# Performance work log

Measured on AMD Instinct MI355X. Metric: run time of the kernel, lower is better.

Reference implementation:

```python
import jax, jax.numpy as jnp
import numpy as np

NEG_SLOPE = 0.2

def _lrelu(x):
    return jax.nn.leaky_relu(x, NEG_SLOPE)

def _seg_mean(vals, seg_ids, num_segments):
    # scatter-mean: sum per segment / count (count clamped to 1 -> zeros for empty nodes,
    # matching torch version where untouched nodes keep new_x == 0)
    s = jax.ops.segment_sum(vals, seg_ids, num_segments=num_segments)
    c = jax.ops.segment_sum(jnp.ones((vals.shape[0], 1), vals.dtype), seg_ids, num_segments=num_segments)
    return s / jnp.maximum(c, 1.0)

def _messages(x, src, dst, rel, ts, rel_emb, time_emb, W_rt, b_rt, W_fc, b_fc):
    # MessagePassing.forward: rel_e = lrelu(rel_t_trans(cat(rel_e, time_e)));
    # m = lrelu(fc(cat(x[src], rel_e, x[dst])))
    rel_e = _lrelu(jnp.concatenate([rel_emb[rel], time_emb[ts]], axis=-1) @ W_rt + b_rt)  # [E, 2h]
    m = _lrelu(jnp.concatenate([x[src], rel_e, x[dst]], axis=-1) @ W_fc + b_fc)           # [E, 2h]
    return m

def setup_inputs() -> dict:
    key = jax.random.key(0)
    ks = jax.random.split(key, 16)
    N, F, H, E, B = 20000, 128, 64, 200000, 256
    NUM_REL, NUM_TS, MAX_ENT = 200, 365, 5000
    s = 0.05
    inp = {}
    inp['x_feat'] = jax.random.normal(ks[0], (N, F), jnp.float32)
    inp['node_grp_emb'] = jax.random.normal(ks[1], (MAX_ENT, H), jnp.float32) * s
    inp['rel_emb'] = jax.random.normal(ks[2], (NUM_REL, H), jnp.float32) * s
    # TimeEncode (TGAT-style fixed frequencies): cos(t * 1/10^(linspace(0,9,H)))
    t = jnp.arange(NUM_TS, dtype=jnp.float32)
    freq = 1.0 / (10.0 ** jnp.linspace(0.0, 9.0, H, dtype=jnp.float32))
    inp['time_emb'] = jnp.cos(t[:, None] * freq[None, :])
    inp['W_node'] = jax.random.normal(ks[3], (F, H), jnp.float32) * s
    inp['b_node'] = jnp.zeros((H,), jnp.float32)
    inp['W_rt'] = jax.random.normal(ks[4], (2 * H, 2 * H), jnp.float32) * s
    inp['b_rt'] = jnp.zeros((2 * H,), jnp.float32)
    inp['W_fc'] = jax.random.normal(ks[5], (6 * H, 2 * H), jnp.float32) * s
    inp['b_fc'] = jnp.zeros((2 * H,), jnp.float32)
    inp['w_pred'] = jax.random.normal(ks[6], (6 * H, 1), jnp.float32) * s
    inp['b_pred'] = jnp.zeros((1,), jnp.float32)
    inp['node_ent'] = jax.random.randint(ks[7], (N,), 0, MAX_ENT)
    inp['edge_src'] = jax.random.randint(ks[8], (E,), 0, N)
    inp['edge_dst'] = jax.random.randint(ks[9], (E,), 0, N)
    inp['edge_type'] = jax.random.randint(ks[10], (E,), 0, NUM_REL)
    inp['edge_ts'] = jax.random.randint(ks[11], (E,), 0, NUM_TS)
    inp['q_s'] = jax.random.randint(ks[12], (B,), 0, N)
    inp['q_o'] = jax.random.randint(ks[13], (B,), 0, N)
    inp['q_r'] = jax.random.randint(ks[14], (B,), 0, NUM_REL)
    inp['q_t'] = jax.random.randint(ks[15], (B,), 0, NUM_TS)
    inp['num_hops'] = 2
    return inp

def reference(x_feat, node_grp_emb, rel_emb, time_emb, W_node, b_node, W_rt, b_rt,
              W_fc, b_fc, w_pred, b_pred, node_ent, edge_src, edge_dst, edge_type,
              edge_ts, q_s, q_o, q_r, q_t, num_hops):
    N = x_feat.shape[0]
    # node init: x = cat(lrelu(node_emb(feat)), node_grp_emb[ent])  (dropout = eval identity)
    x = jnp.concatenate([_lrelu(x_feat @ W_node + b_node), node_grp_emb[node_ent]], axis=-1)  # [N, 2h]
    # multi-hop gather -> edge MLP -> scatter-mean (frontier loop flattened to num_hops full passes)
    for _ in range(num_hops):
        m = _messages(x, edge_src, edge_dst, edge_type, edge_ts, rel_emb, time_emb, W_rt, b_rt, W_fc, b_fc)
        x = x + _seg_mean(m, edge_dst, N)
    # final aggregation only into query destination nodes q_o
    m = _messages(x, edge_src, edge_dst, edge_type, edge_ts, rel_emb, time_emb, W_rt, b_rt, W_fc, b_fc)
    agg = _seg_mean(m, edge_dst, N)
    qo_mask = jnp.zeros((N, 1), x.dtype).at[q_o].set(1.0)
    x = x + agg * qo_mask
    # query relation/time transform and prediction
    q_r_t = _lrelu(jnp.concatenate([rel_emb[q_r], time_emb[q_t]], axis=-1) @ W_rt + b_rt)  # [B, 2h]
    final_feat = jnp.concatenate([x[q_s], q_r_t, x[q_o]], axis=-1)                          # [B, 6h]
    out = jax.nn.sigmoid(final_feat @ w_pred + b_pred)
    return out.squeeze(-1)
```

## Files before the change

### kernel.cpp

```cpp
#include <hip/hip_runtime.h>
#include <cstddef>
#include <cstdint>

#define H 64
#define TWOH 128
#define LRELU(v) ((v) >= 0.f ? (v) : 0.2f * (v))

typedef __attribute__((ext_vector_type(4))) float f32x4;
typedef __attribute__((ext_vector_type(8))) short bf16x8;

__device__ inline unsigned short f2bf(float f) {
    union { float f; unsigned u; } v; v.f = f;
    unsigned u = v.u + 0x7FFFu + ((v.u >> 16) & 1u);
    return (unsigned short)(u >> 16);
}
__device__ inline float bf2f(unsigned u16) {
    union { unsigned u; float f; } v; v.u = u16 << 16; return v.f;
}

__global__ __launch_bounds__(256) void k_setup(
    const float* __restrict__ xf, const float* __restrict__ grp,
    const float* __restrict__ Wn, const float* __restrict__ bn,
    const int* __restrict__ ent, float* __restrict__ x, unsigned short* __restrict__ xb,
    const float* __restrict__ Wfc, unsigned short* __restrict__ WT,
    const float* __restrict__ rel_emb, const float* __restrict__ time_emb,
    const float* __restrict__ Wrt, const float* __restrict__ brt,
    const int* __restrict__ qr, const int* __restrict__ qt,
    float* __restrict__ AR, float* __restrict__ BT, float* __restrict__ qrt,
    const int* __restrict__ dst, int* deg,
    int N, int E, int B, int NUM_REL, int NUM_TS,
    int NB_NI, int NB_TW, int NB_RT)
{
    int b = blockIdx.x, t = threadIdx.x;
    __shared__ float s_u[32][128];
    if (b < NB_NI) {
        int n0 = b * 32;
        int w = t >> 6, l = t & 63;
#pragma unroll
        for (int i = 0; i < 4; ++i) {
            int idx = t + i * 256; int r = idx >> 5, c4 = (idx & 31) * 4;
            int n = n0 + r;
            float4 v = make_float4(0.f, 0.f, 0.f, 0.f);
            if (n < N) v = *(const float4*)(xf + (size_t)n * 128 + c4);
            *(float4*)(&s_u[r][c4]) = v;
        }
        __syncthreads();
        float acc[8];
#pragma unroll
        for (int r = 0; r < 8; ++r) acc[r] = 0.f;
        for (int k = 0; k < 128; ++k) {
            float wv = Wn[k * H + l];
#pragma unroll
            for (int r = 0; r < 8; ++r) acc[r] += s_u[w * 8 + r][k] * wv;
        }
        float bb = bn[l];
        for (int r = 0; r < 8; ++r) {
            int n = n0 + w * 8 + r; if (n >= N) break;
            float v = LRELU(acc[r] + bb);
            float g = grp[(size_t)ent[n] * H + l];
            x[(size_t)n * TWOH + l]      = v;
            x[(size_t)n * TWOH + H + l]  = g;
            xb[(size_t)n * TWOH + l]     = f2bf(v);
            xb[(size_t)n * TWOH + H + l] = f2bf(g);
        }
    } else if (b < NB_NI + NB_TW) {
        int tid = (b - NB_NI) * 256 + t;
        int m = tid >> 14, rem = tid & 16383, col = rem >> 7, k = rem & 127;
        WT[(size_t)m * 16384 + col * 128 + k] = f2bf(Wfc[((size_t)m * 128 + k) * 128 + col]);
    } else if (b < NB_NI + NB_TW + NB_RT) {
        int sub = t >> 7, tt = t & 127;
        int row = (b - NB_NI - NB_TW) * 2 + sub;
        int RT_ROWS = NUM_REL + NUM_TS + B;
        int valid = row < RT_ROWS;
        int type = 0, ridx = 0;
        if (valid) {
            if (row < NUM_REL)               { type = 0; ridx = row; }
            else if (row < NUM_REL + NUM_TS) { type = 1; ridx = row - NUM_REL; }
            else                             { type = 2; ridx = row - NUM_REL - NUM_TS; }
        }
        float lv = 0.f;
        if (valid) {
            if (type == 0)      lv = (tt < H) ? rel_emb[(size_t)ridx * H + tt] : 0.f;
            else if (type == 1) lv = (tt >= H) ? time_emb[(size_t)ridx * H + (tt - H)] : 0.f;
            else                lv = (tt < H) ? rel_emb[(size_t)qr[ridx] * H + tt]
                                              : time_emb[(size_t)qt[ridx] * H + (tt - H)];
        }
        s_u[sub][tt] = lv;
        __syncthreads();
        if (valid) {
            float acc = 0.f;
            for (int k = 0; k < 128; ++k) acc += s_u[sub][k] * Wrt[(size_t)k * TWOH + tt];
            if (type != 1) acc += brt[tt];
            if (type == 2) acc = LRELU(acc);
            if (type == 0)      AR[(size_t)ridx * TWOH + tt]  = acc;
            else if (type == 1) BT[(size_t)ridx * TWOH + tt]  = acc;
            else                qrt[(size_t)ridx * TWOH + tt] = acc;
        }
    } else {
        int e = (b - NB_NI - NB_TW - NB_RT) * 256 + t;
        if (e < E) atomicAdd(&deg[dst[e]], 1);
    }
}

__global__ __launch_bounds__(1024) void k_scan(const int* __restrict__ deg,
                                               int* __restrict__ curs, int N)
{
    __shared__ int wpre[17];
    __shared__ int carry;
    int t = (int)threadIdx.x, wave = t >> 6, lane = t & 63;
    if (t == 0) carry = 0;
    __syncthreads();
    for (int base = 0; base < N; base += 1024) {
        int i = base + t;
        int v = (i < N) ? deg[i] : 0;
        int sv = v;
#pragma unroll
        for (int off = 1; off < 64; off <<= 1) {
            int u = __shfl_up(sv, off);
            if (lane >= off) sv += u;
        }
        if (lane == 63) wpre[wave + 1] = sv;
        __syncthreads();
        if (t == 0) {
            wpre[0] = 0;
            for (int w = 1; w <= 16; ++w) wpre[w] += wpre[w - 1];
        }
        __syncthreads();
        if (i < N) curs[i] = carry + wpre[wave] + sv - v;
        __syncthreads();
        if (t == 0) carry += wpre[16];
        __syncthreads();
    }
}

__global__ __launch_bounds__(256) void k_mid2(
    const float* __restrict__ AR, const float* __restrict__ BT,
    const unsigned short* __restrict__ WT, const float* __restrict__ bd,
    unsigned short* __restrict__ RE2b, int NC, int NUM_TS,
    const unsigned short* __restrict__ xb,
    unsigned short* __restrict__ XSb, unsigned short* __restrict__ XDb, int N,
    const int* __restrict__ src, const int* __restrict__ dst,
    const int* __restrict__ etype, const int* __restrict__ ets,
    int* cursor, int2* __restrict__ a_sc, int E,
    const int* __restrict__ qo, int* maski, int* __restrict__ qlist, int* cntQ, int B,
    int NB_RE2, int NB_G, int NB_SC)
{
    __shared__ __align__(16) char smem[33280];
    int b = blockIdx.x, t = threadIdx.x;
    if (b < NB_RE2) {
        unsigned short* s_mid = (unsigned short*)smem;
        unsigned short* s_out = (unsigned short*)(smem + 16384);
        int* s_rel = (int*)(smem + 32768);
        int* s_ts  = s_rel + 64;
        const unsigned short* WTr = WT + 16384;
        int c0 = b * 64;
        if (t < 64) {
            int cc = c0 + t; if (cc >= NC) cc = NC - 1;
            int rel = cc / NUM_TS;
            s_rel[t] = rel; s_ts[t] = cc - rel * NUM_TS;
        }
        __syncthreads();
#pragma unroll
        for (int i = 0; i < 4; ++i) {
            int idx = t + i * 256;
            int r = idx >> 4, c8 = (idx & 15) * 8;
            const float* ar = AR + (size_t)s_rel[r] * TWOH + c8;
            const float* bt = BT + (size_t)s_ts[r]  * TWOH + c8;
            unsigned short tmp[8] __attribute__((aligned(16)));
#pragma unroll
            for (int j = 0; j < 8; ++j) {
                float v = ar[j] + bt[j];
                tmp[j] = f2bf(LRELU(v));
            }
            int byte = r * 256 + ((c8 * 2) ^ ((r & 7) << 4));
            *(bf16x8*)(smem + byte) = *(bf16x8*)tmp;
        }
        __syncthreads();
        int w = t >> 6, l = t & 63;
        int arow = w * 16 + (l & 15);
        int kgrp = (l >> 4) * 8;
        f32x4 acc[8];
#pragma unroll
        for (int ct = 0; ct < 8; ++ct) acc[ct] = (f32x4){0.f, 0.f, 0.f, 0.f};
#pragma unroll
        for (int kc = 0; kc < 128; kc += 32) {
            int kb = (kc + kgrp) * 2;
            bf16x8 a = *(bf16x8*)((char*)s_mid + arow * 256 + (kb ^ ((arow & 7) << 4)));
#pragma unroll
            for (int ct = 0; ct < 8; ++ct) {
                bf16x8 bb = *(const bf16x8*)(WTr + (size_t)(ct * 16 + (l & 15)) * TWOH + kc + kgrp);
                acc[ct] = __builtin_amdgcn_mfma_f32_16x16x32_bf16(a, bb, acc[ct], 0, 0, 0);
            }
        }
#pragma unroll
        for (int ct = 0; ct < 8; ++ct) {
#pragma unroll
            for (int reg = 0; reg < 4; ++reg) {
                int row  = w * 16 + (l >> 4) * 4 + reg;
                int colb = (ct * 16 + (l & 15)) * 2;
                *(unsigned short*)((char*)s_out + row * 256 + (colb ^ ((row & 7) << 4)))
                    = f2bf(acc[ct][reg]);
            }
        }
        __syncthreads();
#pragma unroll
        for (int i = 0; i < 4; ++i) {
            int idx = t + i * 256;
            int r = idx >> 4, c16 = (idx & 15) * 16;
            int cc = c0 + r;
            if (cc >= NC) continue;
            bf16x8 v = *(bf16x8*)((char*)s_out + r * 256 + (c16 ^ ((r & 7) << 4)));
            *(bf16x8*)(RE2b + (size_t)cc * TWOH + c16 / 2) = v;
        }
    } else if (b < NB_RE2 + NB_G) {
        unsigned short* s_oS = (unsigned short*)smem;
        unsigned short* s_oD = (unsigned short*)(smem + 8192);
        int bid = b - NB_RE2;
        int n0 = (bid >> 1) * 64;
        int colbase = (bid & 1) * 64;
        const unsigned short* WTs = WT;
        const unsigned short* WTd = WT + 32768;
        int w = t >> 6, l = t & 63;
        int node = n0 + w * 16 + (l & 15); if (node >= N) node = N - 1;
        int kgrp = (l >> 4) * 8;
        f32x4 aS[4], aD[4];
#pragma unroll
        for (int ct = 0; ct < 4; ++ct) { aS[ct] = (f32x4){0.f,0.f,0.f,0.f}; aD[ct] = (f32x4){0.f,0.f,0.f,0.f}; }
#pragma unroll
        for (int kc = 0; kc < 128; kc += 32) {
            bf16x8 a = *(const bf16x8*)(xb + (size_t)node * TWOH + kc + kgrp);
#pragma unroll
            for (int ct = 0; ct < 4; ++ct) {
                size_t wo = (size_t)(colbase + ct * 16 + (l & 15)) * TWOH + kc + kgrp;
                bf16x8 b1 = *(const bf16x8*)(WTs + wo);
                bf16x8 b2 = *(const bf16x8*)(WTd + wo);
                aS[ct] = __builtin_amdgcn_mfma_f32_16x16x32_bf16(a, b1, aS[ct], 0, 0, 0);
                aD[ct] = __builtin_amdgcn_mfma_f32_16x16x32_bf16(a, b2, aD[ct], 0, 0, 0);
            }
        }
#pragma unroll
        for (int ct = 0; ct < 4; ++ct) {
            int lc = ct * 16 + (l & 15);
            float bb = bd[colbase + lc];
#pragma unroll
            for (int reg = 0; reg < 4; ++reg) {
                int row = w * 16 + (l >> 4) * 4 + reg;
                int off = row * 128 + ((lc * 2) ^ ((row & 7) << 4));
                *(unsigned short*)((char*)s_oS + off) = f2bf(aS[ct][reg]);
                *(unsigned short*)((char*)s_oD + off) = f2bf(aD[ct][reg] + bb);
            }
        }
        __syncthreads();
#pragma unroll
        for (int i = 0; i < 2; ++i) {
            int idx = t + i * 256;
            int r = idx >> 3, c16 = (idx & 7) * 16;
            int n = n0 + r; if (n >= N) continue;
            int off = r * 128 + (c16 ^ ((r & 7) << 4));
            *(bf16x8*)(XSb + (size_t)n * TWOH + colbase + c16 / 2) = *(bf16x8*)((char*)s_oS + off);
            *(bf16x8*)(XDb + (size_t)n * TWOH + colbase + c16 / 2) = *(bf16x8*)((char*)s_oD + off);
        }
    } else if (b < NB_RE2 + NB_G + NB_SC) {
        int e = (b - NB_RE2 - NB_G) * 256 + t;
        if (e < E) {
            int pos = atomicAdd(&cursor[dst[e]], 1);
            a_sc[pos] = make_int2(src[e], etype[e] * NUM_TS + ets[e]);
        }
    } else {
        for (int i = t; i < B; i += 256) {
            int n = qo[i];
            if (atomicExch(&maski[n], 1) == 0) qlist[atomicAdd(cntQ, 1)] = n;
        }
    }
}

__global__ __launch_bounds__(256) void k_gemm_dual_mfma(
    const unsigned short* __restrict__ xb,
    const unsigned short* __restrict__ WTs, const unsigned short* __restrict__ WTd,
    const float* __restrict__ bd,
    unsigned short* __restrict__ XSb, unsigned short* __restrict__ XDb, int M)
{
    __shared__ unsigned short s_oS[64 * 64];
    __shared__ unsigned short s_oD[64 * 64];
    int t  = threadIdx.x;
    int n0 = blockIdx.x * 64;
    int colbase = blockIdx.y * 64;
    int w = t >> 6, l = t & 63;
    int node = n0 + w * 16 + (l & 15); if (node >= M) node = M - 1;
    int kgrp = (l >> 4) * 8;
    f32x4 aS[4], aD[4];
#pragma unroll
    for (int ct = 0; ct < 4; ++ct) { aS[ct] = (f32x4){0.f,0.f,0.f,0.f}; aD[ct] = (f32x4){0.f,0.f,0.f,0.f}; }
#pragma unroll
    for (int kc = 0; kc < 128; kc += 32) {
        bf16x8 a = *(const bf16x8*)(xb + (size_t)node * TWOH + kc + kgrp);
#pragma unroll
        for (int ct = 0; ct < 4; ++ct) {
            size_t wo = (size_t)(colbase + ct * 16 + (l & 15)) * TWOH + kc + kgrp;
            bf16x8 b1 = *(const bf16x8*)(WTs + wo);
            bf16x8 b2 = *(const bf16x8*)(WTd + wo);
            aS[ct] = __builtin_amdgcn_mfma_f32_16x16x32_bf16(a, b1, aS[ct], 0, 0, 0);
            aD[ct] = __builtin_amdgcn_mfma_f32_16x16x32_bf16(a, b2, aD[ct], 0, 0, 0);
        }
    }
#pragma unroll
    for (int ct = 0; ct < 4; ++ct) {
        int lc = ct * 16 + (l & 15);
        float bb = bd[colbase + lc];
#pragma unroll
        for (int reg = 0; reg < 4; ++reg) {
            int row = w * 16 + (l >> 4) * 4 + reg;
            int off = row * 128 + ((lc * 2) ^ ((row & 7) << 4));
            *(unsigned short*)((char*)s_oS + off) = f2bf(aS[ct][reg]);
            *(unsigned short*)((char*)s_oD + off) = f2bf(aD[ct][reg] + bb);
        }
    }
    __syncthreads();
#pragma unroll
    for (int i = 0; i < 2; ++i) {
        int idx = t + i * 256;
        int r = idx >> 3, c16 = (idx & 7) * 16;
        int n = n0 + r; if (n >= M) continue;
        int off = r * 128 + (c16 ^ ((r & 7) << 4));
        *(bf16x8*)(XSb + (size_t)n * TWOH + colbase + c16 / 2) = *(bf16x8*)((char*)s_oS + off);
        *(bf16x8*)(XDb + (size_t)n * TWOH + colbase + c16 / 2) = *(bf16x8*)((char*)s_oD + off);
    }
}

__global__ __launch_bounds__(256) void k_gemm_list(
    const unsigned short* __restrict__ xb, const unsigned short* __restrict__ WT,
    const float* __restrict__ bd,
    const int* __restrict__ listS, const int* __restrict__ cntS,
    const int* __restrict__ qlist, const int* __restrict__ cntQ,
    unsigned short* __restrict__ XSb, unsigned short* __restrict__ XDb)
{
    int mode = blockIdx.y;
    const int* list = mode ? qlist : listS;
    int c = mode ? *cntQ : *cntS;
    int r0 = blockIdx.x * 64;
    if (r0 >= c) return;
    const unsigned short* W = mode ? (WT + 32768) : WT;
    unsigned short* Out = mode ? XDb : XSb;

    __shared__ unsigned short s_out[64 * 128];
    int t = threadIdx.x;
    int w = t >> 6, l = t & 63;
    int slot = r0 + w * 16 + (l & 15); if (slot >= c) slot = c - 1;
    int node = list[slot];
    int kgrp = (l >> 4) * 8;
    f32x4 acc[8];
#pragma unroll
    for (int ct = 0; ct < 8; ++ct) acc[ct] = (f32x4){0.f, 0.f, 0.f, 0.f};
#pragma unroll
    for (int kc = 0; kc < 128; kc += 32) {
        bf16x8 a = *(const bf16x8*)(xb + (size_t)node * TWOH + kc + kgrp);
#pragma unroll
        for (int ct = 0; ct < 8; ++ct) {
            bf16x8 b = *(const bf16x8*)(W + (size_t)(ct * 16 + (l & 15)) * TWOH + kc + kgrp);
            acc[ct] = __builtin_amdgcn_mfma_f32_16x16x32_bf16(a, b, acc[ct], 0, 0, 0);
        }
    }
#pragma unroll
    for (int ct = 0; ct < 8; ++ct) {
        int col = ct * 16 + (l & 15);
        float bb = mode ? bd[col] : 0.f;
#pragma unroll
        for (int reg = 0; reg < 4; ++reg) {
            int row = w * 16 + (l >> 4) * 4 + reg;
            int off = row * 256 + ((col * 2) ^ ((row & 7) << 4));
            *(unsigned short*)((char*)s_out + off) = f2bf(acc[ct][reg] + bb);
        }
    }
    __syncthreads();
#pragma unroll
    for (int i = 0; i < 4; ++i) {
        int idx = t + i * 256;
        int r = idx >> 4, c16 = (idx & 15) * 16;
        if (r0 + r >= c) continue;
        int n = list[r0 + r];
        bf16x8 v = *(bf16x8*)((char*)s_out + r * 256 + (c16 ^ ((r & 7) << 4)));
        *(bf16x8*)(Out + (size_t)n * TWOH + c16 / 2) = v;
    }
}

__global__ __launch_bounds__(256) void k_agg(
    float* __restrict__ x, unsigned short* __restrict__ xb,
    const unsigned short* __restrict__ XSb, const unsigned short* __restrict__ XDb,
    const unsigned short* __restrict__ RE2b,
    const int* __restrict__ cursor, const int* __restrict__ deg,
    const int2* __restrict__ a_sc,
    const int* __restrict__ list, const int* __restrict__ cnt, int N,
    int nAggBlk, const int* __restrict__ qlistM, const int* __restrict__ cntQM,
    int* maskS, int* __restrict__ listS, int* cntS)
{
    if ((int)blockIdx.x >= nAggBlk) {
        int slot = ((int)blockIdx.x - nAggBlk) * 4 + (threadIdx.x >> 6);
        if (slot >= *cntQM) return;
        int n = qlistM[slot];
        int lane = threadIdx.x & 63;
        int end = cursor[n], start = end - deg[n];
        for (int p = start + lane; p < end; p += 64) {
            int s = a_sc[p].x;
            if (atomicExch(&maskS[s], 1) == 0) listS[atomicAdd(cntS, 1)] = s;
        }
        return;
    }
    int slot = blockIdx.x * 4 + (threadIdx.x >> 6);
    int n;
    if (list) {
        if (slot >= *cnt) return;
        n = list[slot];
    } else {
        n = slot; if (n >= N) return;
    }
    int lane = threadIdx.x & 63;
    int col  = lane * 2;
    int d    = deg[n];
    int end  = cursor[n], start = end - d;
    unsigned cvu = *(const unsigned*)(XDb + (size_t)n * TWOH + col);
    float cvx = bf2f(cvu & 0xFFFFu), cvy = bf2f(cvu >> 16);
    float ax = 0.f, ay = 0.f;
    for (int base = start; base < end; base += 64) {
        int m = end - base; if (m > 64) m = 64;
        int2 my = make_int2(0, 0);
        if (base + lane < end) my = a_sc[base + lane];
        int j = 0;
        for (; j + 4 <= m; j += 4) {
            int s0 = __shfl(my.x, j),     c0 = __shfl(my.y, j);
            int s1 = __shfl(my.x, j + 1), c1 = __shfl(my.y, j + 1);
            int s2 = __shfl(my.x, j + 2), c2 = __shfl(my.y, j + 2);
            int s3 = __shfl(my.x, j + 3), c3 = __shfl(my.y, j + 3);
            unsigned u0 = *(const unsigned*)(XSb  + (size_t)s0 * TWOH + col);
            unsigned v0 = *(const unsigned*)(RE2b + (size_t)c0 * TWOH + col);
            unsigned u1 = *(const unsigned*)(XSb  + (size_t)s1 * TWOH + col);
            unsigned v1 = *(const unsigned*)(RE2b + (size_t)c1 * TWOH + col);
            unsigned u2 = *(const unsigned*)(XSb  + (size_t)s2 * TWOH + col);
            unsigned v2 = *(const unsigned*)(RE2b + (size_t)c2 * TWOH + col);
            unsigned u3 = *(const unsigned*)(XSb  + (size_t)s3 * TWOH + col);
            unsigned v3 = *(const unsigned*)(RE2b + (size_t)c3 * TWOH + col);
            float m0 = bf2f(u0 & 0xFFFFu) + bf2f(v0 & 0xFFFFu) + cvx; m0 = LRELU(m0);
            float m1 = bf2f(u0 >> 16)     + bf2f(v0 >> 16)     + cvy; m1 = LRELU(m1);
            float m2 = bf2f(u1 & 0xFFFFu) + bf2f(v1 & 0xFFFFu) + cvx; m2 = LRELU(m2);
            float m3 = bf2f(u1 >> 16)     + bf2f(v1 >> 16)     + cvy; m3 = LRELU(m3);
            float m4 = bf2f(u2 & 0xFFFFu) + bf2f(v2 & 0xFFFFu) + cvx; m4 = LRELU(m4);
            float m5 = bf2f(u2 >> 16)     + bf2f(v2 >> 16)     + cvy; m5 = LRELU(m5);
            float m6 = bf2f(u3 & 0xFFFFu) + bf2f(v3 & 0xFFFFu) + cvx; m6 = LRELU(m6);
            float m7 = bf2f(u3 >> 16)     + bf2f(v3 >> 16)     + cvy; m7 = LRELU(m7);
            ax += (m0 + m2) + (m4 + m6); ay += (m1 + m3) + (m5 + m7);
        }
        for (; j < m; ++j) {
            int s0 = __shfl(my.x, j), c0 = __shfl(my.y, j);
            unsigned u0 = *(const unsigned*)(XSb  + (size_t)s0 * TWOH + col);
            unsigned v0 = *(const unsigned*)(RE2b + (size_t)c0 * TWOH + col);
            float m0 = bf2f(u0 & 0xFFFFu) + bf2f(v0 & 0xFFFFu) + cvx; m0 = LRELU(m0);
            float m1 = bf2f(u0 >> 16)     + bf2f(v0 >> 16)     + cvy; m1 = LRELU(m1);
            ax += m0; ay += m1;
        }
    }
    float inv = 1.f / (float)(d > 1 ? d : 1);
    float* xr = x + (size_t)n * TWOH + col;
    float nx = xr[0] + ax * inv, ny = xr[1] + ay * inv;
    xr[0] = nx; xr[1] = ny;
    *(unsigned*)(xb + (size_t)n * TWOH + col) = ((unsigned)f2bf(ny) << 16) | f2bf(nx);
}

__global__ __launch_bounds__(64) void k_predict(
    const float* __restrict__ x, const float* __restrict__ qrt,
    const float* __restrict__ wp, const float* __restrict__ bp,
    const int* __restrict__ qs, const int* __restrict__ qo,
    float* __restrict__ out, int B)
{
    int b = blockIdx.x;
    if (b >= B) return;
    int lane = threadIdx.x;
    const float* fs = x + (size_t)qs[b] * TWOH;
    const float* fo = x + (size_t)qo[b] * TWOH;
    const float* fr = qrt + (size_t)b * TWOH;
    float acc = 0.f;
#pragma unroll
    for (int i = 0; i < 2; ++i) {
        int k = lane + i * 64;
        acc += fs[k] * wp[k] + fr[k] * wp[128 + k] + fo[k] * wp[256 + k];
    }
#pragma unroll
    for (int o = 32; o > 0; o >>= 1) acc += __shfl_down(acc, o);
    if (lane == 0) out[b] = 1.f / (1.f + expf(-(acc + bp[0])));
}

extern "C" void kernel_launch(void* const* d_in, const int* in_sizes, int n_in,
                              void* d_out, int out_size, void* d_ws, size_t ws_size,
                              hipStream_t stream)
{
    const float* x_feat   = (const float*)d_in[0];
    const float* grp      = (const float*)d_in[1];
    const float* rel_emb  = (const float*)d_in[2];
    const float* time_emb = (const float*)d_in[3];
    const float* W_node   = (const float*)d_in[4];
    const float* b_node   = (const float*)d_in[5];
    const float* W_rt     = (const float*)d_in[6];
    const float* b_rt     = (const float*)d_in[7];
    const float* W_fc     = (const float*)d_in[8];
    const float* b_fc     = (const float*)d_in[9];
    const float* w_pred   = (const float*)d_in[10];
    const float* b_pred   = (const float*)d_in[11];
    const int* node_ent   = (const int*)d_in[12];
    const int* edge_src   = (const int*)d_in[13];
    const int* edge_dst   = (const int*)d_in[14];
    const int* edge_type  = (const int*)d_in[15];
    const int* edge_ts    = (const int*)d_in[16];
    const int* q_s        = (const int*)d_in[17];
    const int* q_o        = (const int*)d_in[18];
    const int* q_r        = (const int*)d_in[19];
    const int* q_t        = (const int*)d_in[20];
    const int NUM_HOPS = 2;

    int N       = in_sizes[12];
    int E       = in_sizes[13];
    int B       = in_sizes[17];
    int NUM_TS  = in_sizes[3] / H;
    int NUM_REL = in_sizes[2] / H;
    int NC      = NUM_REL * NUM_TS;

    char* ws = (char*)d_ws;
    size_t off = 0;
    auto alloc = [&](size_t bytes) {
        void* p = ws + off; off += (bytes + 255) & ~(size_t)255; return p;
    };
    float*          x    = (float*)         alloc((size_t)N * TWOH * 4);
    unsigned short* xb   = (unsigned short*)alloc((size_t)N * TWOH * 2);
    unsigned short* RE2b = (unsigned short*)alloc((size_t)NC * TWOH * 2);
    unsigned short* XSb  = (unsigned short*)alloc((size_t)N * TWOH * 2);
    unsigned short* XDb  = (unsigned short*)alloc((size_t)N * TWOH * 2);
    unsigned short* WT   = (unsigned short*)alloc((size_t)3 * 128 * 128 * 2);
    float* AR   = (float*)alloc((size_t)NUM_REL * TWOH * 4);
    float* BT   = (float*)alloc((size_t)NUM_TS  * TWOH * 4);
    float* qrt  = (float*)alloc((size_t)B * TWOH * 4);
    int*   degi  = (int*)alloc((size_t)N * 4);
    int*   maski = (int*)alloc((size_t)N * 4);
    int*   maskS = (int*)alloc((size_t)N * 4);
    int*   cnts  = (int*)alloc(256);
    int*   qlist = (int*)alloc((size_t)B * 4);
    int*   listS = (int*)alloc((size_t)N * 4);
    int*   curs  = (int*)alloc((size_t)N * 4);
    int2*  a_sc  = (int2*)alloc((size_t)E * 8);
    (void)ws_size; (void)n_in; (void)out_size;
    int* cntQ = cnts, * cntS = cnts + 1;

    hipMemsetAsync(degi, 0, (size_t)((char*)cnts + 256 - (char*)degi), stream);

    int NB_NI  = (N + 31) / 32;
    int NB_TW  = 192;
    int NB_RT  = (NUM_REL + NUM_TS + B + 1) / 2;
    int NB_SC  = (E + 255) / 256;
    int NB_RE2 = (NC + 63) / 64;
    int NB_G   = ((N + 63) / 64) * 2;
    int NB_AGG = (N + 3) / 4;
    int NB_MS  = (B + 3) / 4;

    k_setup<<<NB_NI + NB_TW + NB_RT + NB_SC, 256, 0, stream>>>(
        x_feat, grp, W_node, b_node, node_ent, x, xb,
        W_fc, WT, rel_emb, time_emb, W_rt, b_rt, q_r, q_t, AR, BT, qrt,
        edge_dst, degi, N, E, B, NUM_REL, NUM_TS, NB_NI, NB_TW, NB_RT);
    k_scan<<<1, 1024, 0, stream>>>(degi, curs, N);
    k_mid2<<<NB_RE2 + NB_G + NB_SC + 1, 256, 0, stream>>>(
        AR, BT, WT, b_fc, RE2b, NC, NUM_TS, xb, XSb, XDb, N,
        edge_src, edge_dst, edge_type, edge_ts, curs, a_sc, E,
        q_o, maski, qlist, cntQ, B, NB_RE2, NB_G, NB_SC);

    k_agg<<<NB_AGG + NB_MS, 256, 0, stream>>>(
        x, xb, XSb, XDb, RE2b, curs, degi, a_sc, nullptr, nullptr, N,
        NB_AGG, qlist, cntQ, maskS, listS, cntS);
    for (int pass = 1; pass < NUM_HOPS; ++pass) {
        dim3 grid((N + 63) / 64, 2);
        k_gemm_dual_mfma<<<grid, 256, 0, stream>>>(
            xb, WT, WT + 32768, b_fc, XSb, XDb, N);
        k_agg<<<NB_AGG, 256, 0, stream>>>(
            x, xb, XSb, XDb, RE2b, curs, degi, a_sc, nullptr, nullptr, N,
            NB_AGG, qlist, cntQ, maskS, listS, cntS);
    }
    {
        dim3 grid((N + 63) / 64, 2);
        k_gemm_list<<<grid, 256, 0, stream>>>(xb, WT, b_fc, listS, cntS, qlist, cntQ,
                                              XSb, XDb);
    }
    k_agg<<<NB_MS, 256, 0, stream>>>(
        x, xb, XSb, XDb, RE2b, curs, degi, a_sc, qlist, cntQ, N,
        NB_MS, qlist, cntQ, maskS, listS, cntS);

    k_predict<<<B, 64, 0, stream>>>(x, qrt, w_pred, b_pred, q_s, q_o, (float*)d_out, B);
}
```

Baseline: 171.2 us.

## Reuse degree-count atomic offsets for CSR fill and widen aggregation gathers

After: 171.8 us. No clear change (+0.3%).

```diff
diff --git a/kernel.cpp b/kernel.cpp
--- a/kernel.cpp
+++ b/kernel.cpp
@@ -27,7 +27,7 @@
     const float* __restrict__ Wrt, const float* __restrict__ brt,
     const int* __restrict__ qr, const int* __restrict__ qt,
     float* __restrict__ AR, float* __restrict__ BT, float* __restrict__ qrt,
-    const int* __restrict__ dst, int* deg,
+    const int* __restrict__ dst, int* deg, int* __restrict__ eoff,
     int N, int E, int B, int NUM_REL, int NUM_TS,
     int NB_NI, int NB_TW, int NB_RT)
 {
@@ -98,7 +98,7 @@
         }
     } else {
         int e = (b - NB_NI - NB_TW - NB_RT) * 256 + t;
-        if (e < E) atomicAdd(&deg[dst[e]], 1);
+        if (e < E) eoff[e] = atomicAdd(&deg[dst[e]], 1);
     }
 }
 
@@ -141,7 +141,8 @@
     unsigned short* __restrict__ XSb, unsigned short* __restrict__ XDb, int N,
     const int* __restrict__ src, const int* __restrict__ dst,
     const int* __restrict__ etype, const int* __restrict__ ets,
-    int* cursor, int2* __restrict__ a_sc, int E,
+    const int* __restrict__ curs, const int* __restrict__ eoff,
+    int2* __restrict__ a_sc, int E,
     const int* __restrict__ qo, int* maski, int* __restrict__ qlist, int* cntQ, int B,
     int NB_RE2, int NB_G, int NB_SC)
 {
@@ -263,7 +264,7 @@
     } else if (b < NB_RE2 + NB_G + NB_SC) {
         int e = (b - NB_RE2 - NB_G) * 256 + t;
         if (e < E) {
-            int pos = atomicAdd(&cursor[dst[e]], 1);
+            int pos = curs[dst[e]] + eoff[e];
             a_sc[pos] = make_int2(src[e], etype[e] * NUM_TS + ets[e]);
         }
     } else {
@@ -398,7 +399,7 @@
         if (slot >= *cntQM) return;
         int n = qlistM[slot];
         int lane = threadIdx.x & 63;
-        int end = cursor[n], start = end - deg[n];
+        int start = cursor[n], end = start + deg[n];
         for (int p = start + lane; p < end; p += 64) {
             int s = a_sc[p].x;
             if (atomicExch(&maskS[s], 1) == 0) listS[atomicAdd(cntS, 1)] = s;
@@ -414,54 +415,64 @@
         n = slot; if (n >= N) return;
     }
     int lane = threadIdx.x & 63;
-    int col  = lane * 2;
+    int half = lane >> 5;
+    int c4   = (lane & 31) * 4;
     int d    = deg[n];
-    int end  = cursor[n], start = end - d;
-    unsigned cvu = *(const unsigned*)(XDb + (size_t)n * TWOH + col);
-    float cvx = bf2f(cvu & 0xFFFFu), cvy = bf2f(cvu >> 16);
-    float ax = 0.f, ay = 0.f;
+    int start = cursor[n], end = start + d;
+    uint2 cvu = *(const uint2*)(XDb + (size_t)n * TWOH + c4);
+    float cv0 = bf2f(cvu.x & 0xFFFFu), cv1 = bf2f(cvu.x >> 16);
+    float cv2 = bf2f(cvu.y & 0xFFFFu), cv3 = bf2f(cvu.y >> 16);
+    float a0 = 0.f, a1 = 0.f, a2 = 0.f, a3 = 0.f;
     for (int base = start; base < end; base += 64) {
         int m = end - base; if (m > 64) m = 64;
         int2 my = make_int2(0, 0);
         if (base + lane < end) my = a_sc[base + lane];
         int j = 0;
         for (; j + 4 <= m; j += 4) {
-            int s0 = __shfl(my.x, j),     c0 = __shfl(my.y, j);
-            int s1 = __shfl(my.x, j + 1), c1 = __shfl(my.y, j + 1);
-            int s2 = __shfl(my.x, j + 2), c2 = __shfl(my.y, j + 2);
-            int s3 = __shfl(my.x, j + 3), c3 = __shfl(my.y, j + 3);
-            unsigned u0 = *(const unsigned*)(XSb  + (size_t)s0 * TWOH + col);
-            unsigned v0 = *(const unsigned*)(RE2b + (size_t)c0 * TWOH + col);
-            unsigned u1 = *(const unsigned*)(XSb  + (size_t)s1 * TWOH + col);
-            unsigned v1 = *(const unsigned*)(RE2b + (size_t)c1 * TWOH + col);
-            unsigned u2 = *(const unsigned*)(XSb  + (size_t)s2 * TWOH + col);
-            unsigned v2 = *(const unsigned*)(RE2b + (size_t)c2 * TWOH + col);
-            unsigned u3 = *(const unsigned*)(XSb  + (size_t)s3 * TWOH + col);
-            unsigned v3 = *(const unsigned*)(RE2b + (size_t)c3 * TWOH + col);
-            float m0 = bf2f(u0 & 0xFFFFu) + bf2f(v0 & 0xFFFFu) + cvx; m0 = LRELU(m0);
-            float m1 = bf2f(u0 >> 16)     + bf2f(v0 >> 16)     + cvy; m1 = LRELU(m1);
-            float m2 = bf2f(u1 & 0xFFFFu) + bf2f(v1 & 0xFFFFu) + cvx; m2 = LRELU(m2);
-            float m3 = bf2f(u1 >> 16)     + bf2f(v1 >> 16)     + cvy; m3 = LRELU(m3);
-            float m4 = bf2f(u2 & 0xFFFFu) + bf2f(v2 & 0xFFFFu) + cvx; m4 = LRELU(m4);
-            float m5 = bf2f(u2 >> 16)     + bf2f(v2 >> 16)     + cvy; m5 = LRELU(m5);
-            float m6 = bf2f(u3 & 0xFFFFu) + bf2f(v3 & 0xFFFFu) + cvx; m6 = LRELU(m6);
-            float m7 = bf2f(u3 >> 16)     + bf2f(v3 >> 16)     + cvy; m7 = LRELU(m7);
-            ax += (m0 + m2) + (m4 + m6); ay += (m1 + m3) + (m5 + m7);
-        }
-        for (; j < m; ++j) {
-            int s0 = __shfl(my.x, j), c0 = __shfl(my.y, j);
-            unsigned u0 = *(const unsigned*)(XSb  + (size_t)s0 * TWOH + col);
-            unsigned v0 = *(const unsigned*)(RE2b + (size_t)c0 * TWOH + col);
-            float m0 = bf2f(u0 & 0xFFFFu) + bf2f(v0 & 0xFFFFu) + cvx; m0 = LRELU(m0);
-            float m1 = bf2f(u0 >> 16)     + bf2f(v0 >> 16)     + cvy; m1 = LRELU(m1);
-            ax += m0; ay += m1;
-        }
-    }
-    float inv = 1.f / (float)(d > 1 ? d : 1);
-    float* xr = x + (size_t)n * TWOH + col;
-    float nx = xr[0] + ax * inv, ny = xr[1] + ay * inv;
-    xr[0] = nx; xr[1] = ny;
-    *(unsigned*)(xb + (size_t)n * TWOH + col) = ((unsigned)f2bf(ny) << 16) | f2bf(nx);
+            int iA = j + half, iB = j + 2 + half;
+            int sA = __shfl(my.x, iA), cA = __shfl(my.y, iA);
+            int sB = __shfl(my.x, iB), cB = __shfl(my.y, iB);
+            uint2 uA = *(const uint2*)(XSb  + (size_t)sA * TWOH + c4);
+            uint2 vA = *(const uint2*)(RE2b + (size_t)cA * TWOH + c4);
+            uint2 uB = *(const uint2*)(XSb  + (size_t)sB * TWOH + c4);
+            uint2 vB = *(const uint2*)(RE2b + (size_t)cB * TWOH + c4);
+            float p0 = bf2f(uA.x & 0xFFFFu) + bf2f(vA.x & 0xFFFFu) + cv0; p0 = LRELU(p0);
+            float p1 = bf2f(uA.x >> 16)     + bf2f(vA.x >> 16)     + cv1; p1 = LRELU(p1);
+            float p2 = bf2f(uA.y & 0xFFFFu) + bf2f(vA.y & 0xFFFFu) + cv2; p2 = LRELU(p2);
+            float p3 = bf2f(uA.y >> 16)     + bf2f(vA.y >> 16)     + cv3; p3 = LRELU(p3);
+            float q0 = bf2f(uB.x & 0xFFFFu) + bf2f(vB.x & 0xFFFFu) + cv0; q0 = LRELU(q0);
+            float q1 = bf2f(uB.x >> 16)     + bf2f(vB.x >> 16)     + cv1; q1 = LRELU(q1);
+            float q2 = bf2f(uB.y & 0xFFFFu) + bf2f(vB.y & 0xFFFFu) + cv2; q2 = LRELU(q2);
+            float q3 = bf2f(uB.y >> 16)     + bf2f(vB.y >> 16)     + cv3; q3 = LRELU(q3);
+            a0 += p0 + q0; a1 += p1 + q1; a2 += p2 + q2; a3 += p3 + q3;
+        }
+        for (; j < m; j += 2) {
+            int iA = j + half;
+            int sA = __shfl(my.x, iA), cA = __shfl(my.y, iA);
+            if (iA < m) {
+                uint2 uA = *(const uint2*)(XSb  + (size_t)sA * TWOH + c4);
+                uint2 vA = *(const uint2*)(RE2b + (size_t)cA * TWOH + c4);
+                float p0 = bf2f(uA.x & 0xFFFFu) + bf2f(vA.x & 0xFFFFu) + cv0; p0 = LRELU(p0);
+                float p1 = bf2f(uA.x >> 16)     + bf2f(vA.x >> 16)     + cv1; p1 = LRELU(p1);
+                float p2 = bf2f(uA.y & 0xFFFFu) + bf2f(vA.y & 0xFFFFu) + cv2; p2 = LRELU(p2);
+                float p3 = bf2f(uA.y >> 16)     + bf2f(vA.y >> 16)     + cv3; p3 = LRELU(p3);
+                a0 += p0; a1 += p1; a2 += p2; a3 += p3;
+            }
+        }
+    }
+    a0 += __shfl_xor(a0, 32); a1 += __shfl_xor(a1, 32);
+    a2 += __shfl_xor(a2, 32); a3 += __shfl_xor(a3, 32);
+    if (half == 0) {
+        float inv = 1.f / (float)(d > 1 ? d : 1);
+        float* xr = x + (size_t)n * TWOH + c4;
+        float4 xv = *(float4*)xr;
+        xv.x += a0 * inv; xv.y += a1 * inv; xv.z += a2 * inv; xv.w += a3 * inv;
+        *(float4*)xr = xv;
+        uint2 xbv;
+        xbv.x = ((unsigned)f2bf(xv.y) << 16) | f2bf(xv.x);
+        xbv.y = ((unsigned)f2bf(xv.w) << 16) | f2bf(xv.z);
+        *(uint2*)(xb + (size_t)n * TWOH + c4) = xbv;
+    }
 }
 
 __global__ __launch_bounds__(64) void k_predict(
@@ -542,6 +553,7 @@
     int*   qlist = (int*)alloc((size_t)B * 4);
     int*   listS = (int*)alloc((size_t)N * 4);
     int*   curs  = (int*)alloc((size_t)N * 4);
+    int*   eoff  = (int*)alloc((size_t)E * 4);
     int2*  a_sc  = (int2*)alloc((size_t)E * 8);
     (void)ws_size; (void)n_in; (void)out_size;
     int* cntQ = cnts, * cntS = cnts + 1;
@@ -560,11 +572,11 @@
     k_setup<<<NB_NI + NB_TW + NB_RT + NB_SC, 256, 0, stream>>>(
         x_feat, grp, W_node, b_node, node_ent, x, xb,
         W_fc, WT, rel_emb, time_emb, W_rt, b_rt, q_r, q_t, AR, BT, qrt,
-        edge_dst, degi, N, E, B, NUM_REL, NUM_TS, NB_NI, NB_TW, NB_RT);
+        edge_dst, degi, eoff, N, E, B, NUM_REL, NUM_TS, NB_NI, NB_TW, NB_RT);
     k_scan<<<1, 1024, 0, stream>>>(degi, curs, N);
     k_mid2<<<NB_RE2 + NB_G + NB_SC + 1, 256, 0, stream>>>(
         AR, BT, WT, b_fc, RE2b, NC, NUM_TS, xb, XSb, XDb, N,
-        edge_src, edge_dst, edge_type, edge_ts, curs, a_sc, E,
+        edge_src, edge_dst, edge_type, edge_ts, curs, eoff, a_sc, E,
         q_o, maski, qlist, cntQ, B, NB_RE2, NB_G, NB_SC);
 
     k_agg<<<NB_AGG + NB_MS, 256, 0, stream>>>(
```
